# Performance work log

Measured on AMD Instinct MI355X. Metric: run time of the kernel, lower is better.

The kernel has to match this reference:

```python
import jax, jax.numpy as jnp
import numpy as np

B, S, D, H = 4, 2048, 1024, 16
DK = D // H  # 64


def setup_inputs() -> dict:
    key = jax.random.key(0)
    ks = jax.random.split(key, 9)
    x = jax.random.normal(ks[0], (B, S, D), dtype=jnp.float32)
    # causal mask, broadcast over batch and heads
    attn_mask = jnp.tril(jnp.ones((S, S), dtype=jnp.int32))[None, None]
    scale = 0.02
    Wq = jax.random.normal(ks[1], (D, D), dtype=jnp.float32) * scale
    Wk = jax.random.normal(ks[2], (D, D), dtype=jnp.float32) * scale
    Wv = jax.random.normal(ks[3], (D, D), dtype=jnp.float32) * scale
    Wo = jax.random.normal(ks[4], (D, D), dtype=jnp.float32) * scale
    bq = jax.random.normal(ks[5], (D,), dtype=jnp.float32) * scale
    bk = jax.random.normal(ks[6], (D,), dtype=jnp.float32) * scale
    bv = jax.random.normal(ks[7], (D,), dtype=jnp.float32) * scale
    bo = jax.random.normal(ks[8], (D,), dtype=jnp.float32) * scale
    return {"x": x, "attn_mask": attn_mask, "Wq": Wq, "bq": bq, "Wk": Wk,
            "bk": bk, "Wv": Wv, "bv": bv, "Wo": Wo, "bo": bo}


def reference(x, attn_mask, Wq, bq, Wk, bk, Wv, bv, Wo, bo):
    b, s, d = x.shape
    # projections -> [b, h, s, dk]
    def proj(W, bias):
        return (x @ W + bias).reshape(b, s, H, DK).transpose(0, 2, 1, 3)
    q = proj(Wq, bq)
    k = proj(Wk, bk)
    v = proj(Wv, bv)
    # scores [b, h, s, s]
    scores = jnp.einsum('bhqd,bhkd->bhqk', q, k) / jnp.sqrt(jnp.float32(DK))
    scores = jnp.where(attn_mask == 0, jnp.float32(-1e9), scores)
    probs = jax.nn.softmax(scores, axis=-1)  # dropout_rate=0 -> identity
    attn_out = jnp.einsum('bhqk,bhkd->bhqd', probs, v)
    # combine heads -> [b, s, d], then output projection
    attn_out = attn_out.transpose(0, 2, 1, 3).reshape(b, s, d)
    return attn_out @ Wo + bo
```

## Files before the change

### kernel.cpp

```cpp
#include <hip/hip_runtime.h>
#include <hip/hip_bf16.h>
#include <stdint.h>

#define S_LEN 2048
#define DMODEL 1024
#define NH 16
#define DK 64
#define BATCH 4
#define KDIM 1024
#define SCQ 0.18033688f

using bf16 = __hip_bfloat16;
using bf162 = __hip_bfloat162;

typedef __bf16 v_bf16x8 __attribute__((ext_vector_type(8)));
typedef short v_s16x4 __attribute__((ext_vector_type(4)));
typedef float v_f32x4 __attribute__((ext_vector_type(4)));

union PackB4 { v_s16x4 v; bf162 h[2]; };

__device__ __forceinline__ void gll16(const void* g, void* l) {
    __builtin_amdgcn_global_load_lds(
        (__attribute__((address_space(1))) unsigned int*)g,
        (__attribute__((address_space(3))) unsigned int*)l, 16, 0, 0);
}

struct alignas(8) BF4 { bf16 a, b, c, d; };

__global__ __launch_bounds__(256) void prep(
    const float* __restrict__ x, bf16* __restrict__ xb,
    const float* __restrict__ W0, const float* __restrict__ W1,
    const float* __restrict__ W2, const float* __restrict__ W3,
    bf16* __restrict__ Wt4)
{
    const int z = blockIdx.z;
    const int t = threadIdx.x;
    if (z == 4) {
        int bid = blockIdx.y * 32 + blockIdx.x;
        size_t base4 = (size_t)bid * 2048 + t;
        #pragma unroll
        for (int j = 0; j < 8; j++) {
            size_t i4 = base4 + j * 256;
            float4 v = *(const float4*)(x + i4 * 4);
            BF4 r;
            r.a = __float2bfloat16(v.x);
            r.b = __float2bfloat16(v.y);
            r.c = __float2bfloat16(v.z);
            r.d = __float2bfloat16(v.w);
            *(BF4*)(xb + i4 * 4) = r;
        }
        return;
    }
    __shared__ float tile[32][33];
    const float* W = (z == 0) ? W0 : (z == 1) ? W1 : (z == 2) ? W2 : W3;
    bf16* Wt = Wt4 + (size_t)z * DMODEL * DMODEL;
    const float sc = (z == 0) ? SCQ : 1.0f;
    int tx = t & 31, ty = t >> 5;
    int k0 = blockIdx.x * 32, n0 = blockIdx.y * 32;
    #pragma unroll
    for (int i = 0; i < 4; i++) {
        int k = k0 + ty + 8 * i;
        tile[ty + 8 * i][tx] = W[(size_t)k * DMODEL + n0 + tx];
    }
    __syncthreads();
    #pragma unroll
    for (int i = 0; i < 4; i++) {
        int n = n0 + ty + 8 * i;
        Wt[(size_t)n * DMODEL + k0 + tx] = __float2bfloat16(tile[tx][ty + 8 * i] * sc);
    }
}

__global__ __launch_bounds__(256) void gemm_qkv(
    const bf16* __restrict__ A, const bf16* __restrict__ Wt4,
    const float* __restrict__ bq, const float* __restrict__ bk,
    const float* __restrict__ bv,
    bf16* __restrict__ Qo, bf16* __restrict__ Ko, bf16* __restrict__ Vto)
{
    __shared__ __align__(16) short lds[16384];
    const int z = blockIdx.z;
    const bf16* Bt = Wt4 + (size_t)z * DMODEL * DMODEL;
    const float* bias = (z == 0) ? bq : (z == 1) ? bk : bv;
    const float bsc = (z == 0) ? SCQ : 1.0f;

    const int t = threadIdx.x;
    const int lane = t & 63;
    const int wave = t >> 6;
    const int quad = lane >> 4;
    const int l15 = lane & 15;
    const int m0 = blockIdx.x * 128;
    const int n0 = blockIdx.y * 128;
    const int wRow = (wave >> 1) * 64;
    const int wCol = (wave & 1) * 64;

    const int r0 = t >> 2, p0 = t & 3;
    const int r1 = (t + 256) >> 2, p1 = (t + 256) & 3;

    const bf16* gA0 = A  + (size_t)(m0 + r0) * KDIM + p0 * 8;
    const bf16* gA1 = A  + (size_t)(m0 + r1) * KDIM + p1 * 8;
    const bf16* gB0 = Bt + (size_t)(n0 + r0) * KDIM + p0 * 8;
    const bf16* gB1 = Bt + (size_t)(n0 + r1) * KDIM + p1 * 8;

    v_f32x4 acc[4][4] = {};

    gll16(gA0, lds + t * 8);
    gll16(gA1, lds + t * 8 + 2048);
    gll16(gB0, lds + 4096 + t * 8);
    gll16(gB1, lds + 4096 + t * 8 + 2048);
    __syncthreads();

    int cur = 0;
    for (int k0 = 0; k0 < KDIM; k0 += 32) {
        if (k0 + 32 < KDIM) {
            short* Ad = lds + (cur ^ 1) * 8192;
            short* Bd = Ad + 4096;
            gll16(gA0 + k0 + 32, Ad + t * 8);
            gll16(gA1 + k0 + 32, Ad + t * 8 + 2048);
            gll16(gB0 + k0 + 32, Bd + t * 8);
            gll16(gB1 + k0 + 32, Bd + t * 8 + 2048);
        }
        const short* As = lds + cur * 8192;
        const short* Bs = As + 4096;
        const short* ArowBase = (z == 2) ? Bs : As;
        const short* BrowBase = (z == 2) ? As : Bs;

        v_bf16x8 af[4], bfr[4];
        #pragma unroll
        for (int mt = 0; mt < 4; mt++) {
            int r = wRow + mt * 16 + l15;
            af[mt] = *(const v_bf16x8*)(ArowBase + r * 32 + quad * 8);
        }
        #pragma unroll
        for (int nt = 0; nt < 4; nt++) {
            int r = wCol + nt * 16 + l15;
            bfr[nt] = *(const v_bf16x8*)(BrowBase + r * 32 + quad * 8);
        }
        __builtin_amdgcn_s_setprio(1);
        #pragma unroll
        for (int mt = 0; mt < 4; mt++)
            #pragma unroll
            for (int nt = 0; nt < 4; nt++)
                acc[mt][nt] = __builtin_amdgcn_mfma_f32_16x16x32_bf16(
                    af[mt], bfr[nt], acc[mt][nt], 0, 0, 0);
        __builtin_amdgcn_s_setprio(0);

        __syncthreads();
        cur ^= 1;
    }

    if (z != 2) {
        bf16* C = (z == 0) ? Qo : Ko;
        float bvv[4];
        #pragma unroll
        for (int nt = 0; nt < 4; nt++)
            bvv[nt] = bias[n0 + wCol + nt * 16 + l15] * bsc;
        #pragma unroll
        for (int mt = 0; mt < 4; mt++)
            #pragma unroll
            for (int nt = 0; nt < 4; nt++)
                #pragma unroll
                for (int r = 0; r < 4; r++) {
                    int row = m0 + wRow + mt * 16 + quad * 4 + r;
                    int col = n0 + wCol + nt * 16 + l15;
                    int b = row >> 11, s = row & (S_LEN - 1);
                    int h = col >> 6, dk = col & (DK - 1);
                    C[(((size_t)(b * NH + h)) * S_LEN + s) * DK + dk] =
                        __float2bfloat16(acc[mt][nt][r] + bvv[nt]);
                }
    } else {
        float bvv[4][4];
        #pragma unroll
        for (int mt = 0; mt < 4; mt++)
            #pragma unroll
            for (int r = 0; r < 4; r++)
                bvv[mt][r] = bias[n0 + wRow + mt * 16 + quad * 4 + r];
        #pragma unroll
        for (int mt = 0; mt < 4; mt++)
            #pragma unroll
            for (int nt = 0; nt < 4; nt++)
                #pragma unroll
                for (int r = 0; r < 4; r++) {
                    int ng = n0 + wRow + mt * 16 + quad * 4 + r;
                    int rowg = m0 + wCol + nt * 16 + l15;
                    int b = rowg >> 11, s = rowg & (S_LEN - 1);
                    int h = ng >> 6, dk = ng & (DK - 1);
                    Vto[(((size_t)(b * NH + h)) * DK + dk) * S_LEN + s] =
                        __float2bfloat16(acc[mt][nt][r] + bvv[mt][r]);
                }
    }
}

__global__ __launch_bounds__(256) void gemm_o(
    const bf16* __restrict__ A, const bf16* __restrict__ Bt,
    const float* __restrict__ bias, float* __restrict__ C)
{
    __shared__ __align__(16) short lds[16384];
    const int t = threadIdx.x;
    const int lane = t & 63;
    const int wave = t >> 6;
    const int quad = lane >> 4;
    const int l15 = lane & 15;
    const int m0 = blockIdx.x * 128;
    const int n0 = blockIdx.y * 128;
    const int wRow = (wave >> 1) * 64;
    const int wCol = (wave & 1) * 64;

    const int r0 = t >> 2, p0 = t & 3;
    const int r1 = (t + 256) >> 2, p1 = (t + 256) & 3;

    const bf16* gA0 = A  + (size_t)(m0 + r0) * KDIM + p0 * 8;
    const bf16* gA1 = A  + (size_t)(m0 + r1) * KDIM + p1 * 8;
    const bf16* gB0 = Bt + (size_t)(n0 + r0) * KDIM + p0 * 8;
    const bf16* gB1 = Bt + (size_t)(n0 + r1) * KDIM + p1 * 8;

    v_f32x4 acc[4][4] = {};

    gll16(gA0, lds + t * 8);
    gll16(gA1, lds + t * 8 + 2048);
    gll16(gB0, lds + 4096 + t * 8);
    gll16(gB1, lds + 4096 + t * 8 + 2048);
    __syncthreads();

    int cur = 0;
    for (int k0 = 0; k0 < KDIM; k0 += 32) {
        if (k0 + 32 < KDIM) {
            short* Ad = lds + (cur ^ 1) * 8192;
            short* Bd = Ad + 4096;
            gll16(gA0 + k0 + 32, Ad + t * 8);
            gll16(gA1 + k0 + 32, Ad + t * 8 + 2048);
            gll16(gB0 + k0 + 32, Bd + t * 8);
            gll16(gB1 + k0 + 32, Bd + t * 8 + 2048);
        }
        const short* As = lds + cur * 8192;
        const short* Bs = As + 4096;

        v_bf16x8 af[4], bfr[4];
        #pragma unroll
        for (int mt = 0; mt < 4; mt++) {
            int r = wRow + mt * 16 + l15;
            af[mt] = *(const v_bf16x8*)(As + r * 32 + quad * 8);
        }
        #pragma unroll
        for (int nt = 0; nt < 4; nt++) {
            int r = wCol + nt * 16 + l15;
            bfr[nt] = *(const v_bf16x8*)(Bs + r * 32 + quad * 8);
        }
        __builtin_amdgcn_s_setprio(1);
        #pragma unroll
        for (int mt = 0; mt < 4; mt++)
            #pragma unroll
            for (int nt = 0; nt < 4; nt++)
                acc[mt][nt] = __builtin_amdgcn_mfma_f32_16x16x32_bf16(
                    af[mt], bfr[nt], acc[mt][nt], 0, 0, 0);
        __builtin_amdgcn_s_setprio(0);

        __syncthreads();
        cur ^= 1;
    }

    float bvv[4];
    #pragma unroll
    for (int nt = 0; nt < 4; nt++) bvv[nt] = bias[n0 + wCol + nt * 16 + l15];

    #pragma unroll
    for (int mt = 0; mt < 4; mt++)
        #pragma unroll
        for (int nt = 0; nt < 4; nt++)
            #pragma unroll
            for (int r = 0; r < 4; r++) {
                int row = m0 + wRow + mt * 16 + quad * 4 + r;
                int col = n0 + wCol + nt * 16 + l15;
                C[(size_t)row * DMODEL + col] = acc[mt][nt][r] + bvv[nt];
            }
}

__global__ __launch_bounds__(256) void attn_mfma(
    const bf16* __restrict__ Qg, const bf16* __restrict__ Kg,
    const bf16* __restrict__ Vtg, bf16* __restrict__ Og)
{
    __shared__ __align__(16) short lds[16384];

    const int t = threadIdx.x;
    const int lane = t & 63;
    const int wave = t >> 6;
    const int quad = lane >> 4;
    const int l15 = lane & 15;
    const int bh = blockIdx.x;
    const int ybal[16] = {15, 8, 7, 0, 14, 9, 6, 1, 13, 10, 5, 2, 12, 11, 4, 3};
    const int by = blockIdx.y;
    const int yy = ybal[(by & 3) * 4 + (by >> 2)];
    const int q0 = yy * 128;
    const int ntiles = 2 * (yy + 1);

    const size_t baseK = (size_t)bh * S_LEN * DK;
    const size_t baseVt = (size_t)bh * DK * S_LEN;

    const int cr = t >> 3;
    const int cs = (t & 7) ^ (cr & 7);
    const bf16* srcK = Kg + baseK + (size_t)cr * DK + cs * 8;
    const bf16* srcV = Vtg + baseVt + (size_t)cr * S_LEN + cs * 8;

    v_bf16x8 qf[2][2];
    #pragma unroll
    for (int qt = 0; qt < 2; qt++) {
        int q = q0 + wave * 32 + qt * 16 + l15;
        #pragma unroll
        for (int kc = 0; kc < 2; kc++)
            qf[qt][kc] = *(const v_bf16x8*)(Qg + baseK + (size_t)q * DK + kc * 32 + quad * 8);
    }

    int vfA[4][4];
    #pragma unroll
    for (int kt = 0; kt < 4; kt++)
        #pragma unroll
        for (int dt = 0; dt < 4; dt++)
            vfA[kt][dt] = ((dt * 16 + l15) * 64 +
                           ((kt * 2 + (quad >> 1)) ^ (l15 & 7)) * 8 +
                           (quad & 1) * 4) * 2 + 8192;

    v_f32x4 oacc[2][4] = {};
    float lrun[2] = {0.f, 0.f};

    {
        short* Kd = lds;
        short* Vd = lds + 4096;
        gll16(srcK, Kd + t * 8);
        gll16(srcK + 32 * DK, Kd + t * 8 + 2048);
        gll16(srcV, Vd + t * 8);
        gll16(srcV + 32 * S_LEN, Vd + t * 8 + 2048);
    }
    __syncthreads();

    int cur = 0;
    for (int tt = 0; tt < ntiles; tt++) {
        if (tt + 1 < ntiles) {
            short* Kd = lds + (cur ^ 1) * 8192;
            short* Vd = Kd + 4096;
            const bf16* sk = srcK + (size_t)(tt + 1) * (64 * DK);
            const bf16* sv = srcV + (size_t)(tt + 1) * 64;
            gll16(sk, Kd + t * 8);
            gll16(sk + 32 * DK, Kd + t * 8 + 2048);
            gll16(sv, Vd + t * 8);
            gll16(sv + 32 * S_LEN, Vd + t * 8 + 2048);
        }
        const int cb = cur << 14;
        const short* Ks = lds + cur * 8192;

        v_f32x4 s_[4][2];
        __builtin_amdgcn_s_setprio(1);
        #pragma unroll
        for (int kt = 0; kt < 4; kt++) {
            int krow = kt * 16 + l15;
            v_bf16x8 kf0 = *(const v_bf16x8*)(Ks + krow * 64 + ((quad) ^ (krow & 7)) * 8);
            v_bf16x8 kf1 = *(const v_bf16x8*)(Ks + krow * 64 + ((4 + quad) ^ (krow & 7)) * 8);
            #pragma unroll
            for (int qt = 0; qt < 2; qt++) {
                v_f32x4 a = {};
                a = __builtin_amdgcn_mfma_f32_16x16x32_bf16(kf0, qf[qt][0], a, 0, 0, 0);
                a = __builtin_amdgcn_mfma_f32_16x16x32_bf16(kf1, qf[qt][1], a, 0, 0, 0);
                s_[kt][qt] = a;
            }
        }
        __builtin_amdgcn_s_setprio(0);

        if (tt >= ntiles - 2) {
            int kbase = (tt - (ntiles - 2)) * 64;
            #pragma unroll
            for (int kt = 0; kt < 4; kt++)
                #pragma unroll
                for (int qt = 0; qt < 2; qt++) {
                    int qq = wave * 32 + qt * 16 + l15;
                    #pragma unroll
                    for (int r = 0; r < 4; r++) {
                        int key = kbase + kt * 16 + quad * 4 + r;
                        if (key > qq) s_[kt][qt][r] = -1e30f;
                    }
                }
        }

        PackB4 pk[4][2];
        #pragma unroll
        for (int kt = 0; kt < 4; kt++)
            #pragma unroll
            for (int qt = 0; qt < 2; qt++) {
                float p0 = __builtin_amdgcn_exp2f(s_[kt][qt][0]);
                float p1 = __builtin_amdgcn_exp2f(s_[kt][qt][1]);
                float p2 = __builtin_amdgcn_exp2f(s_[kt][qt][2]);
                float p3 = __builtin_amdgcn_exp2f(s_[kt][qt][3]);
                lrun[qt] += (p0 + p1) + (p2 + p3);
                pk[kt][qt].h[0] = __float22bfloat162_rn(make_float2(p0, p1));
                pk[kt][qt].h[1] = __float22bfloat162_rn(make_float2(p2, p3));
            }

        __builtin_amdgcn_s_setprio(1);
        #pragma unroll
        for (int kt = 0; kt < 4; kt++) {
            v_s16x4 vf[4];
            #pragma unroll
            for (int dt = 0; dt < 4; dt++)
                vf[dt] = *(const v_s16x4*)((const char*)lds + cb + vfA[kt][dt]);
            #pragma unroll
            for (int qt = 0; qt < 2; qt++)
                #pragma unroll
                for (int dt = 0; dt < 4; dt++)
                    oacc[qt][dt] = __builtin_amdgcn_mfma_f32_16x16x16bf16_1k(
                        vf[dt], pk[kt][qt].v, oacc[qt][dt], 0, 0, 0);
        }
        __builtin_amdgcn_s_setprio(0);

        __syncthreads();
        cur ^= 1;
    }

    #pragma unroll
    for (int qt = 0; qt < 2; qt++) {
        lrun[qt] += __shfl_xor(lrun[qt], 16);
        lrun[qt] += __shfl_xor(lrun[qt], 32);
    }
    #pragma unroll
    for (int qt = 0; qt < 2; qt++) {
        float inv = 1.f / lrun[qt];
        int qloc = wave * 32 + qt * 16 + l15;
        #pragma unroll
        for (int dt = 0; dt < 4; dt++) {
            PackB4 ou;
            ou.h[0] = __float22bfloat162_rn(
                make_float2(oacc[qt][dt][0] * inv, oacc[qt][dt][1] * inv));
            ou.h[1] = __float22bfloat162_rn(
                make_float2(oacc[qt][dt][2] * inv, oacc[qt][dt][3] * inv));
            *(v_s16x4*)(lds + qloc * 72 + dt * 16 + quad * 4) = ou.v;
        }
    }
    __syncthreads();
    {
        const int b = bh >> 4, h = bh & 15;
        int row = t >> 1, half = t & 1;
        size_t gbase = (((size_t)b * S_LEN + q0 + row) * NH + h) * DK + half * 32;
        #pragma unroll
        for (int j = 0; j < 4; j++)
            *(uint4*)(Og + gbase + j * 8) =
                *(const uint4*)(lds + row * 72 + half * 32 + j * 8);
    }
}

extern "C" void kernel_launch(void* const* d_in, const int* in_sizes, int n_in,
                              void* d_out, int out_size, void* d_ws, size_t ws_size,
                              hipStream_t stream) {
    const float* x  = (const float*)d_in[0];
    const float* Wq = (const float*)d_in[2];
    const float* bq = (const float*)d_in[3];
    const float* Wk = (const float*)d_in[4];
    const float* bk = (const float*)d_in[5];
    const float* Wv = (const float*)d_in[6];
    const float* bv = (const float*)d_in[7];
    const float* Wo = (const float*)d_in[8];
    const float* bo = (const float*)d_in[9];
    float* out = (float*)d_out;

    const size_t TEN = (size_t)BATCH * S_LEN * DMODEL * sizeof(bf16);
    char* ws = (char*)d_ws;
    bf16* xb  = (bf16*)ws;
    bf16* Vt  = (bf16*)(ws + TEN);
    bf16* Wt4 = (bf16*)(ws + 2 * TEN);
    bf16* Q   = (bf16*)d_out;
    bf16* Kt  = (bf16*)((char*)d_out + TEN);
    bf16* AO  = xb;

    hipLaunchKernelGGL(prep, dim3(32, 32, 5), dim3(256),
                       0, stream, x, xb, Wq, Wk, Wv, Wo, Wt4);

    hipLaunchKernelGGL(gemm_qkv, dim3(BATCH * S_LEN / 128, DMODEL / 128, 3), dim3(256),
                       0, stream, xb, Wt4, bq, bk, bv, Q, Kt, Vt);

    hipLaunchKernelGGL(attn_mfma, dim3(BATCH * NH, S_LEN / 128), dim3(256),
                       0, stream, Q, Kt, Vt, AO);

    hipLaunchKernelGGL(gemm_o, dim3(BATCH * S_LEN / 128, DMODEL / 128), dim3(256),
                       0, stream, AO, Wt4 + (size_t)3 * DMODEL * DMODEL, bo, out);
}
```

Measured before the change: 258.2 us.

## Pair causal query tiles per block to balance attention work

The attention grid is halved so each block handles two query tiles, yy=15-pr then yy=pr. Every block then processes the same total number of key tiles, replacing the old lookup-table reordering of blocks. The goal is even per-block work and fewer blocks with uneven tails. In exchange, each block runs serially for longer and there are only 512 blocks, so fewer blocks are available to fill the CUs.

```diff
diff --git a/kernel.cpp b/kernel.cpp
--- a/kernel.cpp
+++ b/kernel.cpp
@@ -285,11 +285,7 @@
     const int quad = lane >> 4;
     const int l15 = lane & 15;
     const int bh = blockIdx.x;
-    const int ybal[16] = {15, 8, 7, 0, 14, 9, 6, 1, 13, 10, 5, 2, 12, 11, 4, 3};
-    const int by = blockIdx.y;
-    const int yy = ybal[(by & 3) * 4 + (by >> 2)];
-    const int q0 = yy * 128;
-    const int ntiles = 2 * (yy + 1);
+    const int pr = blockIdx.y;
 
     const size_t baseK = (size_t)bh * S_LEN * DK;
     const size_t baseVt = (size_t)bh * DK * S_LEN;
@@ -299,146 +295,157 @@
     const bf16* srcK = Kg + baseK + (size_t)cr * DK + cs * 8;
     const bf16* srcV = Vtg + baseVt + (size_t)cr * S_LEN + cs * 8;
 
-    v_bf16x8 qf[2][2];
+    int vfA[4][4], kfA[4][2];
     #pragma unroll
-    for (int qt = 0; qt < 2; qt++) {
-        int q = q0 + wave * 32 + qt * 16 + l15;
-        #pragma unroll
-        for (int kc = 0; kc < 2; kc++)
-            qf[qt][kc] = *(const v_bf16x8*)(Qg + baseK + (size_t)q * DK + kc * 32 + quad * 8);
-    }
-
-    int vfA[4][4];
-    #pragma unroll
-    for (int kt = 0; kt < 4; kt++)
+    for (int kt = 0; kt < 4; kt++) {
+        int krow = kt * 16 + l15;
+        kfA[kt][0] = (krow * 64 + ((quad) ^ (krow & 7)) * 8) * 2;
+        kfA[kt][1] = (krow * 64 + ((4 + quad) ^ (krow & 7)) * 8) * 2;
         #pragma unroll
         for (int dt = 0; dt < 4; dt++)
             vfA[kt][dt] = ((dt * 16 + l15) * 64 +
                            ((kt * 2 + (quad >> 1)) ^ (l15 & 7)) * 8 +
                            (quad & 1) * 4) * 2 + 8192;
-
-    v_f32x4 oacc[2][4] = {};
-    float lrun[2] = {0.f, 0.f};
-
-    {
-        short* Kd = lds;
-        short* Vd = lds + 4096;
-        gll16(srcK, Kd + t * 8);
-        gll16(srcK + 32 * DK, Kd + t * 8 + 2048);
-        gll16(srcV, Vd + t * 8);
-        gll16(srcV + 32 * S_LEN, Vd + t * 8 + 2048);
-    }
-    __syncthreads();
-
-    int cur = 0;
-    for (int tt = 0; tt < ntiles; tt++) {
-        if (tt + 1 < ntiles) {
-            short* Kd = lds + (cur ^ 1) * 8192;
-            short* Vd = Kd + 4096;
-            const bf16* sk = srcK + (size_t)(tt + 1) * (64 * DK);
-            const bf16* sv = srcV + (size_t)(tt + 1) * 64;
-            gll16(sk, Kd + t * 8);
-            gll16(sk + 32 * DK, Kd + t * 8 + 2048);
-            gll16(sv, Vd + t * 8);
-            gll16(sv + 32 * S_LEN, Vd + t * 8 + 2048);
-        }
-        const int cb = cur << 14;
-        const short* Ks = lds + cur * 8192;
-
-        v_f32x4 s_[4][2];
-        __builtin_amdgcn_s_setprio(1);
-        #pragma unroll
-        for (int kt = 0; kt < 4; kt++) {
-            int krow = kt * 16 + l15;
-            v_bf16x8 kf0 = *(const v_bf16x8*)(Ks + krow * 64 + ((quad) ^ (krow & 7)) * 8);
-            v_bf16x8 kf1 = *(const v_bf16x8*)(Ks + krow * 64 + ((4 + quad) ^ (krow & 7)) * 8);
-            #pragma unroll
-            for (int qt = 0; qt < 2; qt++) {
-                v_f32x4 a = {};
-                a = __builtin_amdgcn_mfma_f32_16x16x32_bf16(kf0, qf[qt][0], a, 0, 0, 0);
-                a = __builtin_amdgcn_mfma_f32_16x16x32_bf16(kf1, qf[qt][1], a, 0, 0, 0);
-                s_[kt][qt] = a;
-            }
-        }
-        __builtin_amdgcn_s_setprio(0);
-
-        if (tt >= ntiles - 2) {
-            int kbase = (tt - (ntiles - 2)) * 64;
+    }
+
+    #pragma unroll 1
+    for (int half = 0; half < 2; half++) {
+        const int yy = half ? pr : 15 - pr;
+        const int q0 = yy * 128;
+        const int ntiles = 2 * (yy + 1);
+
+        v_bf16x8 qf[2][2];
+        #pragma unroll
+        for (int qt = 0; qt < 2; qt++) {
+            int q = q0 + wave * 32 + qt * 16 + l15;
+            #pragma unroll
+            for (int kc = 0; kc < 2; kc++)
+                qf[qt][kc] = *(const v_bf16x8*)(Qg + baseK + (size_t)q * DK +
+                                                kc * 32 + quad * 8);
+        }
+
+        v_f32x4 oacc[2][4] = {};
+        float lrun[2] = {0.f, 0.f};
+
+        __syncthreads();
+        {
+            short* Kd = lds;
+            short* Vd = lds + 4096;
+            gll16(srcK, Kd + t * 8);
+            gll16(srcK + 32 * DK, Kd + t * 8 + 2048);
+            gll16(srcV, Vd + t * 8);
+            gll16(srcV + 32 * S_LEN, Vd + t * 8 + 2048);
+        }
+        __syncthreads();
+
+        int cur = 0;
+        for (int tt = 0; tt < ntiles; tt++) {
+            if (tt + 1 < ntiles) {
+                short* Kd = lds + (cur ^ 1) * 8192;
+                short* Vd = Kd + 4096;
+                const bf16* sk = srcK + (size_t)(tt + 1) * (64 * DK);
+                const bf16* sv = srcV + (size_t)(tt + 1) * 64;
+                gll16(sk, Kd + t * 8);
+                gll16(sk + 32 * DK, Kd + t * 8 + 2048);
+                gll16(sv, Vd + t * 8);
+                gll16(sv + 32 * S_LEN, Vd + t * 8 + 2048);
+            }
+            const int cb = cur << 14;
+
+            v_f32x4 s_[4][2];
+            __builtin_amdgcn_s_setprio(1);
+            #pragma unroll
+            for (int kt = 0; kt < 4; kt++) {
+                v_bf16x8 kf0 = *(const v_bf16x8*)((const char*)lds + cb + kfA[kt][0]);
+                v_bf16x8 kf1 = *(const v_bf16x8*)((const char*)lds + cb + kfA[kt][1]);
+                #pragma unroll
+                for (int qt = 0; qt < 2; qt++) {
+                    v_f32x4 a = {};
+                    a = __builtin_amdgcn_mfma_f32_16x16x32_bf16(kf0, qf[qt][0], a, 0, 0, 0);
+                    a = __builtin_amdgcn_mfma_f32_16x16x32_bf16(kf1, qf[qt][1], a, 0, 0, 0);
+                    s_[kt][qt] = a;
+                }
+            }
+            __builtin_amdgcn_s_setprio(0);
+
+            if (tt >= ntiles - 2) {
+                int kbase = (tt - (ntiles - 2)) * 64;
+                #pragma unroll
+                for (int kt = 0; kt < 4; kt++)
+                    #pragma unroll
+                    for (int qt = 0; qt < 2; qt++) {
+                        int qq = wave * 32 + qt * 16 + l15;
+                        #pragma unroll
+                        for (int r = 0; r < 4; r++) {
+                            int key = kbase + kt * 16 + quad * 4 + r;
+                            if (key > qq) s_[kt][qt][r] = -1e30f;
+                        }
+                    }
+            }
+
+            PackB4 pk[4][2];
             #pragma unroll
             for (int kt = 0; kt < 4; kt++)
                 #pragma unroll
                 for (int qt = 0; qt < 2; qt++) {
-                    int qq = wave * 32 + qt * 16 + l15;
+                    float p0 = __builtin_amdgcn_exp2f(s_[kt][qt][0]);
+                    float p1 = __builtin_amdgcn_exp2f(s_[kt][qt][1]);
+                    float p2 = __builtin_amdgcn_exp2f(s_[kt][qt][2]);
+                    float p3 = __builtin_amdgcn_exp2f(s_[kt][qt][3]);
+                    lrun[qt] += (p0 + p1) + (p2 + p3);
+                    pk[kt][qt].h[0] = __float22bfloat162_rn(make_float2(p0, p1));
+                    pk[kt][qt].h[1] = __float22bfloat162_rn(make_float2(p2, p3));
+                }
+
+            __builtin_amdgcn_s_setprio(1);
+            #pragma unroll
+            for (int kt = 0; kt < 4; kt++) {
+                v_s16x4 vf[4];
+                #pragma unroll
+                for (int dt = 0; dt < 4; dt++)
+                    vf[dt] = *(const v_s16x4*)((const char*)lds + cb + vfA[kt][dt]);
+                #pragma unroll
+                for (int qt = 0; qt < 2; qt++)
                     #pragma unroll
-                    for (int r = 0; r < 4; r++) {
-                        int key = kbase + kt * 16 + quad * 4 + r;
-                        if (key > qq) s_[kt][qt][r] = -1e30f;
-                    }
-                }
-        }
-
-        PackB4 pk[4][2];
-        #pragma unroll
-        for (int kt = 0; kt < 4; kt++)
-            #pragma unroll
-            for (int qt = 0; qt < 2; qt++) {
-                float p0 = __builtin_amdgcn_exp2f(s_[kt][qt][0]);
-                float p1 = __builtin_amdgcn_exp2f(s_[kt][qt][1]);
-                float p2 = __builtin_amdgcn_exp2f(s_[kt][qt][2]);
-                float p3 = __builtin_amdgcn_exp2f(s_[kt][qt][3]);
-                lrun[qt] += (p0 + p1) + (p2 + p3);
-                pk[kt][qt].h[0] = __float22bfloat162_rn(make_float2(p0, p1));
-                pk[kt][qt].h[1] = __float22bfloat162_rn(make_float2(p2, p3));
-            }
-
-        __builtin_amdgcn_s_setprio(1);
-        #pragma unroll
-        for (int kt = 0; kt < 4; kt++) {
-            v_s16x4 vf[4];
-            #pragma unroll
-            for (int dt = 0; dt < 4; dt++)
-                vf[dt] = *(const v_s16x4*)((const char*)lds + cb + vfA[kt][dt]);
-            #pragma unroll
-            for (int qt = 0; qt < 2; qt++)
-                #pragma unroll
-                for (int dt = 0; dt < 4; dt++)
-                    oacc[qt][dt] = __builtin_amdgcn_mfma_f32_16x16x16bf16_1k(
-                        vf[dt], pk[kt][qt].v, oacc[qt][dt], 0, 0, 0);
-        }
-        __builtin_amdgcn_s_setprio(0);
-
+                    for (int dt = 0; dt < 4; dt++)
+                        oacc[qt][dt] = __builtin_amdgcn_mfma_f32_16x16x16bf16_1k(
+                            vf[dt], pk[kt][qt].v, oacc[qt][dt], 0, 0, 0);
+            }
+            __builtin_amdgcn_s_setprio(0);
+
+            __syncthreads();
+            cur ^= 1;
+        }
+
+        #pragma unroll
+        for (int qt = 0; qt < 2; qt++) {
+            lrun[qt] += __shfl_xor(lrun[qt], 16);
+            lrun[qt] += __shfl_xor(lrun[qt], 32);
+        }
+        #pragma unroll
+        for (int qt = 0; qt < 2; qt++) {
+            float inv = 1.f / lrun[qt];
+            int qloc = wave * 32 + qt * 16 + l15;
+            #pragma unroll
+            for (int dt = 0; dt < 4; dt++) {
+                PackB4 ou;
+                ou.h[0] = __float22bfloat162_rn(
+                    make_float2(oacc[qt][dt][0] * inv, oacc[qt][dt][1] * inv));
+                ou.h[1] = __float22bfloat162_rn(
+                    make_float2(oacc[qt][dt][2] * inv, oacc[qt][dt][3] * inv));
+                *(v_s16x4*)(lds + qloc * 72 + dt * 16 + quad * 4) = ou.v;
+            }
+        }
         __syncthreads();
-        cur ^= 1;
-    }
-
-    #pragma unroll
-    for (int qt = 0; qt < 2; qt++) {
-        lrun[qt] += __shfl_xor(lrun[qt], 16);
-        lrun[qt] += __shfl_xor(lrun[qt], 32);
-    }
-    #pragma unroll
-    for (int qt = 0; qt < 2; qt++) {
-        float inv = 1.f / lrun[qt];
-        int qloc = wave * 32 + qt * 16 + l15;
-        #pragma unroll
-        for (int dt = 0; dt < 4; dt++) {
-            PackB4 ou;
-            ou.h[0] = __float22bfloat162_rn(
-                make_float2(oacc[qt][dt][0] * inv, oacc[qt][dt][1] * inv));
-            ou.h[1] = __float22bfloat162_rn(
-                make_float2(oacc[qt][dt][2] * inv, oacc[qt][dt][3] * inv));
-            *(v_s16x4*)(lds + qloc * 72 + dt * 16 + quad * 4) = ou.v;
-        }
-    }
-    __syncthreads();
-    {
-        const int b = bh >> 4, h = bh & 15;
-        int row = t >> 1, half = t & 1;
-        size_t gbase = (((size_t)b * S_LEN + q0 + row) * NH + h) * DK + half * 32;
-        #pragma unroll
-        for (int j = 0; j < 4; j++)
-            *(uint4*)(Og + gbase + j * 8) =
-                *(const uint4*)(lds + row * 72 + half * 32 + j * 8);
+        {
+            const int b = bh >> 4, h = bh & 15;
+            int row = t >> 1, hf = t & 1;
+            size_t gbase = (((size_t)b * S_LEN + q0 + row) * NH + h) * DK + hf * 32;
+            #pragma unroll
+            for (int j = 0; j < 4; j++)
+                *(uint4*)(Og + gbase + j * 8) =
+                    *(const uint4*)(lds + row * 72 + hf * 32 + j * 8);
+        }
     }
 }
 
@@ -471,7 +478,7 @@
     hipLaunchKernelGGL(gemm_qkv, dim3(BATCH * S_LEN / 128, DMODEL / 128, 3), dim3(256),
                        0, stream, xb, Wt4, bq, bk, bv, Q, Kt, Vt);
 
-    hipLaunchKernelGGL(attn_mfma, dim3(BATCH * NH, S_LEN / 128), dim3(256),
+    hipLaunchKernelGGL(attn_mfma, dim3(BATCH * NH, 8), dim3(256),
                        0, stream, Q, Kt, Vt, AO);
 
     hipLaunchKernelGGL(gemm_o, dim3(BATCH * S_LEN / 128, DMODEL / 128), dim3(256),
```

Measured after the change: 272.5 us. 1.06x slower.

## Triple-buffer LDS in projection GEMMs with one barrier per k-step

Applied to the files above, without the earlier changes.

Both projection GEMMs go from a double-buffered LDS ring to a three-stage ring. Each k-step issues the next tile's async global-to-LDS loads, waits only on the previous tile's loads with a partial vmcnt, and uses a single s_barrier instead of two __syncthreads. This is meant to cut barrier stalls and overlap loads with MFMA work. In exchange, LDS per block grows from 32KB to 48KB, which may lower occupancy.

```diff
diff --git a/kernel.cpp b/kernel.cpp
--- a/kernel.cpp
+++ b/kernel.cpp
@@ -76,7 +76,7 @@
     const float* __restrict__ bv,
     bf16* __restrict__ Qo, bf16* __restrict__ Ko, bf16* __restrict__ Vto)
 {
-    __shared__ __align__(16) short lds[16384];
+    __shared__ __align__(16) short lds[24576];
     const int z = blockIdx.z;
     const bf16* Bt = Wt4 + (size_t)z * DMODEL * DMODEL;
     const float* bias = (z == 0) ? bq : (z == 1) ? bk : bv;
@@ -106,19 +106,24 @@
     gll16(gA1, lds + t * 8 + 2048);
     gll16(gB0, lds + 4096 + t * 8);
     gll16(gB1, lds + 4096 + t * 8 + 2048);
-    __syncthreads();
-
-    int cur = 0;
+
+    int rb = 0, sb = 1;
     for (int k0 = 0; k0 < KDIM; k0 += 32) {
         if (k0 + 32 < KDIM) {
-            short* Ad = lds + (cur ^ 1) * 8192;
-            short* Bd = Ad + 4096;
-            gll16(gA0 + k0 + 32, Ad + t * 8);
-            gll16(gA1 + k0 + 32, Ad + t * 8 + 2048);
-            gll16(gB0 + k0 + 32, Bd + t * 8);
-            gll16(gB1 + k0 + 32, Bd + t * 8 + 2048);
-        }
-        const short* As = lds + cur * 8192;
+            short* Sd = lds + sb * 8192;
+            gll16(gA0 + k0 + 32, Sd + t * 8);
+            gll16(gA1 + k0 + 32, Sd + t * 8 + 2048);
+            gll16(gB0 + k0 + 32, Sd + 4096 + t * 8);
+            gll16(gB1 + k0 + 32, Sd + 4096 + t * 8 + 2048);
+            asm volatile("s_waitcnt vmcnt(4)" ::: "memory");
+        } else {
+            asm volatile("s_waitcnt vmcnt(0)" ::: "memory");
+        }
+        __builtin_amdgcn_sched_barrier(0);
+        __builtin_amdgcn_s_barrier();
+        __builtin_amdgcn_sched_barrier(0);
+
+        const short* As = lds + rb * 8192;
         const short* Bs = As + 4096;
         const short* ArowBase = (z == 2) ? Bs : As;
         const short* BrowBase = (z == 2) ? As : Bs;
@@ -143,8 +148,8 @@
                     af[mt], bfr[nt], acc[mt][nt], 0, 0, 0);
         __builtin_amdgcn_s_setprio(0);
 
-        __syncthreads();
-        cur ^= 1;
+        rb = (rb == 2) ? 0 : rb + 1;
+        sb = (sb == 2) ? 0 : sb + 1;
     }
 
     if (z != 2) {
@@ -193,7 +198,7 @@
     const bf16* __restrict__ A, const bf16* __restrict__ Bt,
     const float* __restrict__ bias, float* __restrict__ C)
 {
-    __shared__ __align__(16) short lds[16384];
+    __shared__ __align__(16) short lds[24576];
     const int t = threadIdx.x;
     const int lane = t & 63;
     const int wave = t >> 6;
@@ -218,19 +223,24 @@
     gll16(gA1, lds + t * 8 + 2048);
     gll16(gB0, lds + 4096 + t * 8);
     gll16(gB1, lds + 4096 + t * 8 + 2048);
-    __syncthreads();
-
-    int cur = 0;
+
+    int rb = 0, sb = 1;
     for (int k0 = 0; k0 < KDIM; k0 += 32) {
         if (k0 + 32 < KDIM) {
-            short* Ad = lds + (cur ^ 1) * 8192;
-            short* Bd = Ad + 4096;
-            gll16(gA0 + k0 + 32, Ad + t * 8);
-            gll16(gA1 + k0 + 32, Ad + t * 8 + 2048);
-            gll16(gB0 + k0 + 32, Bd + t * 8);
-            gll16(gB1 + k0 + 32, Bd + t * 8 + 2048);
-        }
-        const short* As = lds + cur * 8192;
+            short* Sd = lds + sb * 8192;
+            gll16(gA0 + k0 + 32, Sd + t * 8);
+            gll16(gA1 + k0 + 32, Sd + t * 8 + 2048);
+            gll16(gB0 + k0 + 32, Sd + 4096 + t * 8);
+            gll16(gB1 + k0 + 32, Sd + 4096 + t * 8 + 2048);
+            asm volatile("s_waitcnt vmcnt(4)" ::: "memory");
+        } else {
+            asm volatile("s_waitcnt vmcnt(0)" ::: "memory");
+        }
+        __builtin_amdgcn_sched_barrier(0);
+        __builtin_amdgcn_s_barrier();
+        __builtin_amdgcn_sched_barrier(0);
+
+        const short* As = lds + rb * 8192;
         const short* Bs = As + 4096;
 
         v_bf16x8 af[4], bfr[4];
@@ -253,8 +263,8 @@
                     af[mt], bfr[nt], acc[mt][nt], 0, 0, 0);
         __builtin_amdgcn_s_setprio(0);
 
-        __syncthreads();
-        cur ^= 1;
+        rb = (rb == 2) ? 0 : rb + 1;
+        sb = (sb == 2) ? 0 : sb + 1;
     }
 
     float bvv[4];
```

Result: no change. 260.4 us (+0.8%).
